# Performance work log

Measured on AMD Instinct MI355X. Metric: run time of the kernel, lower is better.

## Reference

```python
import jax, jax.numpy as jnp
import numpy as np

H = 4          # num attention heads
C1 = 64        # channel_num[0]
C2 = 128       # channel_num[1]
KV = C1 + C2   # 192
MLP = C1 * 4   # expand_ratio=4


def _layernorm(x, g, b, eps=1e-6):
    m = jnp.mean(x, axis=-1, keepdims=True)
    v = jnp.mean((x - m) ** 2, axis=-1, keepdims=True)
    return (x - m) * jax.lax.rsqrt(v + eps) * g + b


def setup_inputs() -> dict:
    key = jax.random.key(0)
    ks = jax.random.split(key, 12)
    B, N = 8, 3136
    s_q = 1.0 / np.sqrt(C1)
    s_kv = 1.0 / np.sqrt(KV)
    return {
        "emb1": jax.random.normal(ks[0], (B, N, C1), jnp.float32),
        "emb2": jax.random.normal(ks[1], (B, N, C2), jnp.float32),
        # per-head projection weights (nn.Linear convention: y = x @ W.T)
        "Wq": jax.random.uniform(ks[2], (H, C1, C1), jnp.float32, -s_q, s_q),
        "Wk": jax.random.uniform(ks[3], (H, KV, KV), jnp.float32, -s_kv, s_kv),
        "Wv": jax.random.uniform(ks[4], (H, KV, KV), jnp.float32, -s_kv, s_kv),
        "Wout": jax.random.uniform(ks[5], (C1, C1), jnp.float32, -s_q, s_q),
        "ln1_g": jnp.ones((C1,), jnp.float32),
        "ln1_b": jnp.zeros((C1,), jnp.float32),
        "lnall_g": jnp.ones((KV,), jnp.float32),
        "lnall_b": jnp.zeros((KV,), jnp.float32),
        "ffn_g": jnp.ones((C1,), jnp.float32),
        "ffn_b": jnp.zeros((C1,), jnp.float32),
        "fc1_w": jax.random.uniform(ks[6], (MLP, C1), jnp.float32, -s_q, s_q),
        "fc1_b": jnp.zeros((MLP,), jnp.float32),
        "fc2_w": jax.random.uniform(ks[7], (C1, MLP), jnp.float32, -1.0 / np.sqrt(MLP), 1.0 / np.sqrt(MLP)),
        "fc2_b": jnp.zeros((C1,), jnp.float32),
    }


def reference(emb1, emb2, Wq, Wk, Wv, Wout, ln1_g, ln1_b, lnall_g, lnall_b,
              ffn_g, ffn_b, fc1_w, fc1_b, fc2_w, fc2_b):
    # emb1: [B,N,C1], emb2: [B,N,C2]
    emb_all = jnp.concatenate([emb1, emb2], axis=2)          # [B,N,KV]
    cx1 = _layernorm(emb1, ln1_g, ln1_b)                     # [B,N,C1]
    ea = _layernorm(emb_all, lnall_g, lnall_b)               # [B,N,KV]

    # batched per-head projections (replaces Python loop over ModuleList)
    qT = jnp.einsum('bnc,hdc->bhdn', cx1, Wq)                # [B,H,C1,N]
    k = jnp.einsum('bnk,hdk->bhnd', ea, Wk)                  # [B,H,N,KV]
    vT = jnp.einsum('bnk,hdk->bhdn', ea, Wv)                 # [B,H,KV,N]

    scores = jnp.einsum('bhcn,bhnk->bhck', qT, k) / np.sqrt(KV)  # [B,H,C1,KV]
    # InstanceNorm2d over spatial dims (C1, KV) per (batch, head), affine=False
    m = jnp.mean(scores, axis=(2, 3), keepdims=True)
    v = jnp.mean((scores - m) ** 2, axis=(2, 3), keepdims=True)
    scores = (scores - m) * jax.lax.rsqrt(v + 1e-5)
    probs = jax.nn.softmax(scores, axis=3)                   # softmax over KV

    ctx = jnp.einsum('bhck,bhkn->bhcn', probs, vT)           # [B,H,C1,N]
    ctx = jnp.mean(ctx, axis=1).transpose(0, 2, 1)           # mean over heads -> [B,N,C1]
    o = ctx @ Wout.T                                         # [B,N,C1]

    cx = emb1 + o                                            # residual
    x = _layernorm(cx, ffn_g, ffn_b)
    x = jax.nn.gelu(x @ fc1_w.T + fc1_b, approximate=False)
    x = x @ fc2_w.T + fc2_b
    return x + cx
```

## Files before the change

kernel.cpp:

```cpp
#include <hip/hip_runtime.h>
#include <hip/hip_bf16.h>

typedef __hip_bfloat16 bf;
typedef unsigned short ushort_t;
typedef __attribute__((ext_vector_type(8))) short short8;
typedef __attribute__((ext_vector_type(4))) float f32x4;

#define NB 8
#define SEQ 3136
#define HD 4
#define ZS 6

__device__ __forceinline__ float lo_bf(unsigned u){ return __uint_as_float(u << 16); }
__device__ __forceinline__ float hi_bf(unsigned u){ return __uint_as_float(u & 0xffff0000u); }
__device__ __forceinline__ float b16f(ushort_t s){ return __uint_as_float(((unsigned)s) << 16); }
__device__ __forceinline__ unsigned short f2bfbits(float f){
  unsigned u = __float_as_uint(f);
  unsigned r = u + 0x7fffu + ((u >> 16) & 1u);
  return (unsigned short)(r >> 16);
}
__device__ __forceinline__ float ldin(const void* p, long i, bool isbf){
  return isbf ? __bfloat162float(((const bf*)p)[i]) : ((const float*)p)[i];
}
__device__ __forceinline__ ushort_t cvt1(const void* p, long i, bool isbf){
  return isbf ? ((const ushort_t*)p)[i] : f2bfbits(((const float*)p)[i]);
}
#define DTYPE_FLAG(p) (((const unsigned*)(p))[0] == 0x3F803F80u)

__device__ __forceinline__ float wsum(float v){
  #pragma unroll
  for (int o = 32; o > 0; o >>= 1) v += __shfl_xor(v, o, 64);
  return v;
}

__global__ __launch_bounds__(512) void k_g(
    const void* __restrict__ emb1, const void* __restrict__ emb2,
    const void* __restrict__ g1, const void* __restrict__ b1,
    const void* __restrict__ ga, const void* __restrict__ ba,
    const void* __restrict__ Wq, const void* __restrict__ Wk, const void* __restrict__ Wv,
    const void* __restrict__ f1w, const void* __restrict__ f2w, const void* __restrict__ Wout,
    ushort_t* __restrict__ part, ushort_t* __restrict__ eag,
    ushort_t* __restrict__ Wqb, ushort_t* __restrict__ Wkb, ushort_t* __restrict__ WvTb,
    ushort_t* __restrict__ f1wb, ushort_t* __restrict__ f2wb,
    ushort_t* __restrict__ Woutb, unsigned* __restrict__ cnt){
  bool isbf = DTYPE_FLAG(g1);
  int tid = threadIdx.x;
  int b = blockIdx.y, ch = blockIdx.x;
  if (ch >= 49){
    if (b != 0) return;
    int g = (ch - 49)*512 + tid;
    const int STR = 24*512;
    if (g < 8) cnt[g] = 0;
    for (int i = g; i < 16384; i += STR) Wqb[i] = cvt1(Wq, i, isbf);
    for (int i = g; i < 4096;  i += STR) Woutb[i] = cvt1(Wout, i, isbf);
    for (int i = g; i < 147456; i += STR) Wkb[i] = cvt1(Wk, i, isbf);
    for (int i = g; i < 147456; i += STR){
      int hh = i / 36864, r = i - hh*36864;
      int j = r / 192, e = r - j*192;
      WvTb[i] = cvt1(Wv, (long)hh*36864 + e*192 + j, isbf);
    }
    for (int i = g; i < 16384; i += STR) f1wb[i] = cvt1(f1w, i, isbf);
    for (int i = g; i < 16384; i += STR) f2wb[i] = cvt1(f2w, i, isbf);
    return;
  }
  __shared__ __align__(16) ushort_t z1t[64*72];
  __shared__ __align__(16) ushort_t zat[192*72];
  int wave = tid >> 6, lane = tid & 63;
  int quad = lane >> 4, nl = lane & 15;
  long t0 = (long)b*SEQ + ch*64;
  float g1l = ldin(g1,lane,isbf), b1l = ldin(b1,lane,isbf);
  float ga0 = ldin(ga,lane,isbf),     ba0 = ldin(ba,lane,isbf);
  float ga1 = ldin(ga,64+lane,isbf),  ba1 = ldin(ba,64+lane,isbf);
  float ga2 = ldin(ga,128+lane,isbf), ba2 = ldin(ba,128+lane,isbf);
  #pragma unroll 4
  for (int k = 0; k < 8; ++k){
    int tok = wave*8 + k;
    long t = t0 + tok;
    float e1  = ldin(emb1, t*64 + lane, isbf);
    float e2a = ldin(emb2, t*128 + lane, isbf);
    float e2b = ldin(emb2, t*128 + 64 + lane, isbf);
    float s1 = wsum(e1), ss1 = wsum(e1*e1);
    float m1 = s1*(1.f/64.f);
    float r1 = rsqrtf(fmaxf(ss1*(1.f/64.f) - m1*m1, 0.f) + 1e-6f);
    z1t[lane*72 + tok] = f2bfbits((e1 - m1)*r1*g1l + b1l);
    float s23 = wsum(e2a+e2b), ss23 = wsum(e2a*e2a + e2b*e2b);
    float ma = (s1+s23)*(1.f/192.f);
    float ra = rsqrtf(fmaxf((ss1+ss23)*(1.f/192.f) - ma*ma, 0.f) + 1e-6f);
    unsigned short za0 = f2bfbits((e1  - ma)*ra*ga0 + ba0);
    unsigned short za1 = f2bfbits((e2a - ma)*ra*ga1 + ba1);
    unsigned short za2 = f2bfbits((e2b - ma)*ra*ga2 + ba2);
    zat[lane*72 + tok]       = za0;
    zat[(64+lane)*72 + tok]  = za1;
    zat[(128+lane)*72 + tok] = za2;
    eag[t*192 + lane]       = za0;
    eag[t*192 + 64 + lane]  = za1;
    eag[t*192 + 128 + lane] = za2;
  }
  __syncthreads();
  int half = wave >> 2, cq = wave & 3;
  short8 a0 = *reinterpret_cast<const short8*>(&z1t[(cq*16+nl)*72 + quad*8]);
  short8 a1 = *reinterpret_cast<const short8*>(&z1t[(cq*16+nl)*72 + 32 + quad*8]);
  ushort_t* P = part + ((long)b*49 + ch)*12288;
  #pragma unroll
  for (int ntl = 0; ntl < 6; ++ntl){
    int nt = half*6 + ntl;
    f32x4 cd = {0.f,0.f,0.f,0.f};
    short8 b0 = *reinterpret_cast<const short8*>(&zat[(nt*16+nl)*72 + quad*8]);
    cd = __builtin_amdgcn_mfma_f32_16x16x32_bf16(a0, b0, cd, 0, 0, 0);
    short8 b1v = *reinterpret_cast<const short8*>(&zat[(nt*16+nl)*72 + 32 + quad*8]);
    cd = __builtin_amdgcn_mfma_f32_16x16x32_bf16(a1, b1v, cd, 0, 0, 0);
    #pragma unroll
    for (int reg = 0; reg < 4; ++reg)
      P[(cq*16 + quad*4 + reg)*192 + nt*16 + nl] = f2bfbits(cd[reg]);
  }
}

__global__ __launch_bounds__(64) void k_red(
    const ushort_t* __restrict__ part, ushort_t* __restrict__ Gb){
  int idx4 = blockIdx.x*64 + threadIdx.x;
  int b = idx4 / 3072, e4 = idx4 - b*3072;
  const ushort_t* p = part + (long)b*49*12288 + e4*4;
  float s0=0.f, s1=0.f, s2=0.f, s3=0.f;
  #pragma unroll
  for (int ch = 0; ch < 49; ++ch){
    uint2 u = *reinterpret_cast<const uint2*>(p + (long)ch*12288);
    s0 += lo_bf(u.x); s1 += hi_bf(u.x); s2 += lo_bf(u.y); s3 += hi_bf(u.y);
  }
  unsigned lo = (unsigned)f2bfbits(s0) | ((unsigned)f2bfbits(s1) << 16);
  unsigned hi = (unsigned)f2bfbits(s2) | ((unsigned)f2bfbits(s3) << 16);
  *reinterpret_cast<uint2*>(Gb + (long)idx4*4) = make_uint2(lo, hi);
}

__global__ __launch_bounds__(256) void k_att(
    const ushort_t* __restrict__ Gb, const ushort_t* __restrict__ Wqb,
    const ushort_t* __restrict__ Wkb, const ushort_t* __restrict__ WvTb,
    const ushort_t* __restrict__ Woutb,
    float* __restrict__ Mh, unsigned* __restrict__ cnt, ushort_t* __restrict__ W2){
  __shared__ __align__(16) ushort_t sT[192*72];
  __shared__ __align__(16) ushort_t sPh[64*200];
  __shared__ __align__(16) ushort_t sPl[64*200];
  __shared__ float red[8];
  __shared__ float stat[2];
  __shared__ unsigned sOld;
  int h = blockIdx.x, b = blockIdx.y, z = blockIdx.z;
  int tid = threadIdx.x, wave = tid >> 6, lane = tid & 63;
  int quad = lane >> 4, nl = lane & 15;

  const ushort_t* Gp = Gb + (long)b*12288;
  short8 aG[6];
  #pragma unroll
  for (int ks = 0; ks < 6; ++ks)
    aG[ks] = *reinterpret_cast<const short8*>(Gp + (wave*16+nl)*192 + ks*32 + quad*8);
  const ushort_t* Wkp = Wkb + (long)h*36864;
  short8 bcur[6], bnxt[6];
  #pragma unroll
  for (int ks = 0; ks < 6; ++ks)
    bcur[ks] = *reinterpret_cast<const short8*>(Wkp + (long)nl*192 + ks*32 + quad*8);
  #pragma unroll
  for (int nt = 0; nt < 12; ++nt){
    if (nt < 11){
      #pragma unroll
      for (int ks = 0; ks < 6; ++ks)
        bnxt[ks] = *reinterpret_cast<const short8*>(Wkp + (long)((nt+1)*16+nl)*192 + ks*32 + quad*8);
    }
    f32x4 cd = {0.f,0.f,0.f,0.f};
    #pragma unroll
    for (int ks = 0; ks < 6; ++ks)
      cd = __builtin_amdgcn_mfma_f32_16x16x32_bf16(aG[ks], bcur[ks], cd, 0, 0, 0);
    #pragma unroll
    for (int reg = 0; reg < 4; ++reg)
      sT[(nt*16+nl)*72 + wave*16 + quad*4 + reg] = f2bfbits(cd[reg]);
    #pragma unroll
    for (int ks = 0; ks < 6; ++ks) bcur[ks] = bnxt[ks];
  }
  __syncthreads();

  const ushort_t* Wqp = Wqb + (long)h*4096;
  short8 aQ[2];
  #pragma unroll
  for (int ks = 0; ks < 2; ++ks)
    aQ[ks] = *reinterpret_cast<const short8*>(Wqp + (wave*16+nl)*64 + ks*32 + quad*8);
  const float scale = 0.07216878364870323f;
  float sv[12][4];
  float ps = 0.f, pss = 0.f;
  #pragma unroll
  for (int nt = 0; nt < 12; ++nt){
    f32x4 cd = {0.f,0.f,0.f,0.f};
    #pragma unroll
    for (int ks = 0; ks < 2; ++ks){
      short8 bt = *reinterpret_cast<const short8*>(&sT[(nt*16+nl)*72 + ks*32 + quad*8]);
      cd = __builtin_amdgcn_mfma_f32_16x16x32_bf16(aQ[ks], bt, cd, 0, 0, 0);
    }
    #pragma unroll
    for (int reg = 0; reg < 4; ++reg){
      float v = cd[reg]*scale;
      sv[nt][reg] = v;
      ps += v; pss += v*v;
    }
  }
  ps = wsum(ps); pss = wsum(pss);
  if (lane == 0){ red[wave] = ps; red[4+wave] = pss; }
  __syncthreads();
  if (tid == 0){
    float s  = red[0]+red[1]+red[2]+red[3];
    float s2 = red[4]+red[5]+red[6]+red[7];
    float m = s * (1.f/12288.f);
    stat[0] = m;
    stat[1] = rsqrtf(fmaxf(s2*(1.f/12288.f) - m*m, 0.f) + 1e-5f);
  }
  __syncthreads();

  const ushort_t* Wvp = WvTb + (long)h*36864;
  short8 bv[2][6];
  #pragma unroll
  for (int ntl = 0; ntl < 2; ++ntl)
    #pragma unroll
    for (int ks = 0; ks < 6; ++ks)
      bv[ntl][ks] = *reinterpret_cast<const short8*>(Wvp + (long)((z*2+ntl)*16+nl)*192 + ks*32 + quad*8);

  float m = stat[0], r = stat[1];
  #pragma unroll
  for (int reg = 0; reg < 4; ++reg){
    float mx = -3.4e38f;
    #pragma unroll
    for (int nt = 0; nt < 12; ++nt){
      float v = (sv[nt][reg] - m)*r;
      sv[nt][reg] = v;
      mx = fmaxf(mx, v);
    }
    #pragma unroll
    for (int o = 1; o < 16; o <<= 1) mx = fmaxf(mx, __shfl_xor(mx, o, 64));
    float sum = 0.f;
    #pragma unroll
    for (int nt = 0; nt < 12; ++nt){
      float e = __expf(sv[nt][reg] - mx);
      sv[nt][reg] = e;
      sum += e;
    }
    #pragma unroll
    for (int o = 1; o < 16; o <<= 1) sum += __shfl_xor(sum, o, 64);
    float inv = 1.f / sum;
    int row = wave*16 + quad*4 + reg;
    #pragma unroll
    for (int nt = 0; nt < 12; ++nt){
      float e = sv[nt][reg]*inv;
      ushort_t hi = f2bfbits(e);
      sPh[row*200 + nt*16 + nl] = hi;
      sPl[row*200 + nt*16 + nl] = f2bfbits(e - b16f(hi));
    }
  }
  __syncthreads();

  short8 aPh[6], aPl[6];
  #pragma unroll
  for (int ks = 0; ks < 6; ++ks){
    aPh[ks] = *reinterpret_cast<const short8*>(&sPh[(wave*16+nl)*200 + ks*32 + quad*8]);
    aPl[ks] = *reinterpret_cast<const short8*>(&sPl[(wave*16+nl)*200 + ks*32 + quad*8]);
  }
  float* Mb = Mh + ((long)b*HD + h)*12288;
  #pragma unroll
  for (int ntl = 0; ntl < 2; ++ntl){
    int nt = z*2 + ntl;
    f32x4 cdh = {0.f,0.f,0.f,0.f};
    f32x4 cdl = {0.f,0.f,0.f,0.f};
    #pragma unroll
    for (int ks = 0; ks < 6; ++ks){
      cdl = __builtin_amdgcn_mfma_f32_16x16x32_bf16(aPl[ks], bv[ntl][ks], cdl, 0, 0, 0);
      cdh = __builtin_amdgcn_mfma_f32_16x16x32_bf16(aPh[ks], bv[ntl][ks], cdh, 0, 0, 0);
    }
    #pragma unroll
    for (int reg = 0; reg < 4; ++reg)
      Mb[(wave*16 + quad*4 + reg)*192 + nt*16 + nl] = cdh[reg] + cdl[reg];
  }

  __threadfence();
  if (tid == 0) sOld = atomicAdd(&cnt[b], 1u);
  __syncthreads();
  if (sOld == HD*ZS - 1u){
    __threadfence();
    const float* M0 = Mh + (long)b*HD*12288;
    for (int g = tid; g < 3072; g += 256){
      float4 x0 = ((const float4*)M0)[g];
      float4 x1 = ((const float4*)(M0 + 12288))[g];
      float4 x2 = ((const float4*)(M0 + 24576))[g];
      float4 x3 = ((const float4*)(M0 + 36864))[g];
      int e = g*4; int c = e/192, j = e - c*192;
      sT[(j+0)*72 + c] = f2bfbits(0.25f*(x0.x+x1.x+x2.x+x3.x));
      sT[(j+1)*72 + c] = f2bfbits(0.25f*(x0.y+x1.y+x2.y+x3.y));
      sT[(j+2)*72 + c] = f2bfbits(0.25f*(x0.z+x1.z+x2.z+x3.z));
      sT[(j+3)*72 + c] = f2bfbits(0.25f*(x0.w+x1.w+x2.w+x3.w));
    }
    __syncthreads();
    short8 aW[2];
    #pragma unroll
    for (int ks = 0; ks < 2; ++ks)
      aW[ks] = *reinterpret_cast<const short8*>(Woutb + (wave*16+nl)*64 + ks*32 + quad*8);
    ushort_t* W2b = W2 + (long)b*12288;
    #pragma unroll
    for (int nt = 0; nt < 12; ++nt){
      f32x4 cd = {0.f,0.f,0.f,0.f};
      #pragma unroll
      for (int ks = 0; ks < 2; ++ks){
        short8 bm = *reinterpret_cast<const short8*>(&sT[(nt*16+nl)*72 + ks*32 + quad*8]);
        cd = __builtin_amdgcn_mfma_f32_16x16x32_bf16(aW[ks], bm, cd, 0, 0, 0);
      }
      #pragma unroll
      for (int reg = 0; reg < 4; ++reg)
        W2b[(wave*16 + quad*4 + reg)*192 + nt*16 + nl] = f2bfbits(cd[reg]);
    }
  }
}

__global__ __launch_bounds__(256) void k_tail(
    const void* __restrict__ emb1, const ushort_t* __restrict__ eag,
    const ushort_t* __restrict__ W2g,
    const void* __restrict__ ffg, const void* __restrict__ ffb,
    const ushort_t* __restrict__ f1wb, const void* __restrict__ f1b,
    const ushort_t* __restrict__ f2wb, const void* __restrict__ f2b,
    const void* __restrict__ lng, void* __restrict__ out){
  bool isbf = DTYPE_FLAG(lng);
  __shared__ __align__(16) ushort_t sCX[16*72];
  __shared__ __align__(16) ushort_t sX[16*88];
  __shared__ __align__(16) ushort_t sH[16*280];
  int tid = threadIdx.x, wave = tid >> 6, lane = tid & 63;
  int quad = lane >> 4, nl = lane & 15;
  int b = blockIdx.y;
  long tbase = (long)b*SEQ + blockIdx.x*16;

  short8 aO[6];
  #pragma unroll
  for (int kt = 0; kt < 6; ++kt)
    aO[kt] = *reinterpret_cast<const short8*>(eag + (tbase + nl)*192 + kt*32 + quad*8);
  const ushort_t* W2b = W2g + (long)b*12288;
  {
    f32x4 cd = {0.f,0.f,0.f,0.f};
    #pragma unroll
    for (int kt = 0; kt < 6; ++kt){
      short8 bf8 = *reinterpret_cast<const short8*>(W2b + (wave*16+nl)*192 + kt*32 + quad*8);
      cd = __builtin_amdgcn_mfma_f32_16x16x32_bf16(aO[kt], bf8, cd, 0, 0, 0);
    }
    #pragma unroll
    for (int reg = 0; reg < 4; ++reg){
      int tokl = quad*4 + reg;
      int chn = wave*16 + nl;
      float e1v = ldin(emb1, (tbase + tokl)*64 + chn, isbf);
      sCX[tokl*72 + chn] = f2bfbits(cd[reg] + e1v);
    }
  }
  __syncthreads();

  float gl = ldin(ffg, lane, isbf), bl = ldin(ffb, lane, isbf);
  #pragma unroll
  for (int k = 0; k < 4; ++k){
    int tokl = wave*4 + k;
    float c = b16f(sCX[tokl*72 + lane]);
    float s = wsum(c), ss = wsum(c*c);
    float m = s*(1.f/64.f);
    float r = rsqrtf(fmaxf(ss*(1.f/64.f) - m*m, 0.f) + 1e-6f);
    sX[tokl*88 + lane] = f2bfbits((c - m)*r*gl + bl);
  }
  __syncthreads();

  short8 aX[2];
  #pragma unroll
  for (int kt = 0; kt < 2; ++kt)
    aX[kt] = *reinterpret_cast<const short8*>(&sX[nl*88 + kt*32 + quad*8]);
  #pragma unroll
  for (int nn = 0; nn < 4; ++nn){
    int nt = wave*4 + nn;
    f32x4 cd = {0.f,0.f,0.f,0.f};
    #pragma unroll
    for (int kt = 0; kt < 2; ++kt){
      short8 bf8 = *reinterpret_cast<const short8*>(f1wb + (long)(nt*16+nl)*64 + kt*32 + quad*8);
      cd = __builtin_amdgcn_mfma_f32_16x16x32_bf16(aX[kt], bf8, cd, 0, 0, 0);
    }
    float bb = ldin(f1b, nt*16+nl, isbf);
    #pragma unroll
    for (int reg = 0; reg < 4; ++reg){
      float v = cd[reg] + bb;
      float h = 0.5f*v*(1.f + erff(v*0.70710678118654752f));
      sH[(quad*4 + reg)*280 + nt*16 + nl] = f2bfbits(h);
    }
  }
  __syncthreads();

  short8 aH[8];
  #pragma unroll
  for (int kt = 0; kt < 8; ++kt)
    aH[kt] = *reinterpret_cast<const short8*>(&sH[nl*280 + kt*32 + quad*8]);
  {
    f32x4 cd = {0.f,0.f,0.f,0.f};
    #pragma unroll
    for (int kt = 0; kt < 8; ++kt){
      short8 bf8 = *reinterpret_cast<const short8*>(f2wb + (long)(wave*16+nl)*256 + kt*32 + quad*8);
      cd = __builtin_amdgcn_mfma_f32_16x16x32_bf16(aH[kt], bf8, cd, 0, 0, 0);
    }
    float bb2 = ldin(f2b, wave*16+nl, isbf);
    #pragma unroll
    for (int reg = 0; reg < 4; ++reg){
      int tokl = quad*4 + reg;
      int chn = wave*16 + nl;
      float y = cd[reg] + bb2 + b16f(sCX[tokl*72 + chn]);
      if (isbf) sCX[tokl*72 + chn] = f2bfbits(y);
      else ((float*)out)[(tbase + tokl)*64 + chn] = y;
    }
  }
  if (isbf){
    __syncthreads();
    int tokl = wave*4 + (lane >> 4), prt = lane & 15;
    uint2 v = *reinterpret_cast<const uint2*>(&sCX[tokl*72 + prt*4]);
    *reinterpret_cast<uint2*>((ushort_t*)out + (tbase + tokl)*64 + prt*4) = v;
  }
}

extern "C" void kernel_launch(void* const* d_in, const int* in_sizes, int n_in,
                              void* d_out, int out_size, void* d_ws, size_t ws_size,
                              hipStream_t stream){
  const void* emb1 = d_in[0];
  const void* emb2 = d_in[1];
  const void* Wq   = d_in[2];
  const void* Wk   = d_in[3];
  const void* Wv   = d_in[4];
  const void* Wout = d_in[5];
  const void* ln1g = d_in[6];
  const void* ln1b = d_in[7];
  const void* lag  = d_in[8];
  const void* lab  = d_in[9];
  const void* ffg  = d_in[10];
  const void* ffb  = d_in[11];
  const void* f1w  = d_in[12];
  const void* f1b  = d_in[13];
  const void* f2w  = d_in[14];
  const void* f2b  = d_in[15];

  char* base = (char*)d_ws;
  ushort_t* part = (ushort_t*)base;
  ushort_t* ea   = (ushort_t*)(base + 9633792);
  ushort_t* Gb   = (ushort_t*)(base + 19267584);
  float*    Mh   = (float*)(base + 19464192);
  ushort_t* W2   = (ushort_t*)(base + 21037056);
  ushort_t* Wqb  = (ushort_t*)(base + 21233664);
  ushort_t* Wkb  = (ushort_t*)(base + 21266432);
  ushort_t* WvTb = (ushort_t*)(base + 21561344);
  ushort_t* f1wb = (ushort_t*)(base + 21856256);
  ushort_t* f2wb = (ushort_t*)(base + 21889024);
  ushort_t* Woutb= (ushort_t*)(base + 21921792);
  unsigned* cnt  = (unsigned*)(base + 21929984);

  k_g   <<<dim3(73,NB),     512, 0, stream>>>(emb1, emb2, ln1g, ln1b, lag, lab,
                                              Wq, Wk, Wv, f1w, f2w, Wout,
                                              part, ea, Wqb, Wkb, WvTb, f1wb, f2wb,
                                              Woutb, cnt);
  k_red <<<384,              64, 0, stream>>>(part, Gb);
  k_att <<<dim3(HD,NB,ZS),  256, 0, stream>>>(Gb, Wqb, Wkb, WvTb, Woutb, Mh, cnt, W2);
  k_tail<<<dim3(196,NB),    256, 0, stream>>>(emb1, ea, W2, ffg, ffb,
                                              f1wb, f1b, f2wb, f2b, ln1g, d_out);
}
```

Before: 183.1 us.

## Split Wout projection out of attention kernel into separate k_w2 launch

```diff
diff --git a/kernel.cpp b/kernel.cpp
--- a/kernel.cpp
+++ b/kernel.cpp
@@ -22,6 +22,14 @@
 __device__ __forceinline__ float ldin(const void* p, long i, bool isbf){
   return isbf ? __bfloat162float(((const bf*)p)[i]) : ((const float*)p)[i];
 }
+__device__ __forceinline__ float4 ld4(const void* p, long i, bool isbf){
+  if (isbf){
+    uint2 u = *reinterpret_cast<const uint2*>((const unsigned short*)p + i);
+    return make_float4(lo_bf(u.x), hi_bf(u.x), lo_bf(u.y), hi_bf(u.y));
+  }
+  const float* f = (const float*)p + i;
+  return make_float4(f[0], f[1], f[2], f[3]);
+}
 __device__ __forceinline__ ushort_t cvt1(const void* p, long i, bool isbf){
   return isbf ? ((const ushort_t*)p)[i] : f2bfbits(((const float*)p)[i]);
 }
@@ -38,11 +46,10 @@
     const void* __restrict__ g1, const void* __restrict__ b1,
     const void* __restrict__ ga, const void* __restrict__ ba,
     const void* __restrict__ Wq, const void* __restrict__ Wk, const void* __restrict__ Wv,
-    const void* __restrict__ f1w, const void* __restrict__ f2w, const void* __restrict__ Wout,
+    const void* __restrict__ f1w, const void* __restrict__ f2w,
     ushort_t* __restrict__ part, ushort_t* __restrict__ eag,
     ushort_t* __restrict__ Wqb, ushort_t* __restrict__ Wkb, ushort_t* __restrict__ WvTb,
-    ushort_t* __restrict__ f1wb, ushort_t* __restrict__ f2wb,
-    ushort_t* __restrict__ Woutb, unsigned* __restrict__ cnt){
+    ushort_t* __restrict__ f1wb, ushort_t* __restrict__ f2wb){
   bool isbf = DTYPE_FLAG(g1);
   int tid = threadIdx.x;
   int b = blockIdx.y, ch = blockIdx.x;
@@ -50,9 +57,7 @@
     if (b != 0) return;
     int g = (ch - 49)*512 + tid;
     const int STR = 24*512;
-    if (g < 8) cnt[g] = 0;
     for (int i = g; i < 16384; i += STR) Wqb[i] = cvt1(Wq, i, isbf);
-    for (int i = g; i < 4096;  i += STR) Woutb[i] = cvt1(Wout, i, isbf);
     for (int i = g; i < 147456; i += STR) Wkb[i] = cvt1(Wk, i, isbf);
     for (int i = g; i < 147456; i += STR){
       int hh = i / 36864, r = i - hh*36864;
@@ -134,14 +139,12 @@
 __global__ __launch_bounds__(256) void k_att(
     const ushort_t* __restrict__ Gb, const ushort_t* __restrict__ Wqb,
     const ushort_t* __restrict__ Wkb, const ushort_t* __restrict__ WvTb,
-    const ushort_t* __restrict__ Woutb,
-    float* __restrict__ Mh, unsigned* __restrict__ cnt, ushort_t* __restrict__ W2){
+    float* __restrict__ Mh){
   __shared__ __align__(16) ushort_t sT[192*72];
   __shared__ __align__(16) ushort_t sPh[64*200];
   __shared__ __align__(16) ushort_t sPl[64*200];
   __shared__ float red[8];
   __shared__ float stat[2];
-  __shared__ unsigned sOld;
   int h = blockIdx.x, b = blockIdx.y, z = blockIdx.z;
   int tid = threadIdx.x, wave = tid >> 6, lane = tid & 63;
   int quad = lane >> 4, nl = lane & 15;
@@ -272,43 +275,50 @@
     for (int reg = 0; reg < 4; ++reg)
       Mb[(wave*16 + quad*4 + reg)*192 + nt*16 + nl] = cdh[reg] + cdl[reg];
   }
-
-  __threadfence();
-  if (tid == 0) sOld = atomicAdd(&cnt[b], 1u);
-  __syncthreads();
-  if (sOld == HD*ZS - 1u){
-    __threadfence();
-    const float* M0 = Mh + (long)b*HD*12288;
-    for (int g = tid; g < 3072; g += 256){
-      float4 x0 = ((const float4*)M0)[g];
-      float4 x1 = ((const float4*)(M0 + 12288))[g];
-      float4 x2 = ((const float4*)(M0 + 24576))[g];
-      float4 x3 = ((const float4*)(M0 + 36864))[g];
-      int e = g*4; int c = e/192, j = e - c*192;
-      sT[(j+0)*72 + c] = f2bfbits(0.25f*(x0.x+x1.x+x2.x+x3.x));
-      sT[(j+1)*72 + c] = f2bfbits(0.25f*(x0.y+x1.y+x2.y+x3.y));
-      sT[(j+2)*72 + c] = f2bfbits(0.25f*(x0.z+x1.z+x2.z+x3.z));
-      sT[(j+3)*72 + c] = f2bfbits(0.25f*(x0.w+x1.w+x2.w+x3.w));
-    }
-    __syncthreads();
-    short8 aW[2];
-    #pragma unroll
-    for (int ks = 0; ks < 2; ++ks)
-      aW[ks] = *reinterpret_cast<const short8*>(Woutb + (wave*16+nl)*64 + ks*32 + quad*8);
-    ushort_t* W2b = W2 + (long)b*12288;
-    #pragma unroll
-    for (int nt = 0; nt < 12; ++nt){
-      f32x4 cd = {0.f,0.f,0.f,0.f};
+}
+
+__global__ __launch_bounds__(256) void k_w2(
+    const float* __restrict__ Mh, const void* __restrict__ Wout,
+    const void* __restrict__ lng, ushort_t* __restrict__ W2){
+  bool isbf = DTYPE_FLAG(lng);
+  __shared__ __align__(16) float sM[64*49];
+  int jc = blockIdx.x, b = blockIdx.y;
+  int tid = threadIdx.x;
+  for (int idx = tid; idx < 3072; idx += 256){
+    int c = idx/48, j = idx - c*48;
+    long base = (long)b*HD*12288 + c*192 + jc*48 + j;
+    float s = Mh[base] + Mh[base+12288] + Mh[base+2*12288] + Mh[base+3*12288];
+    sM[c*49 + j] = 0.25f*s;
+  }
+  __syncthreads();
+  int ty = tid >> 4, tx = tid & 15;
+  float acc[4][3];
+  #pragma unroll
+  for (int i=0;i<4;++i) for (int q=0;q<3;++q) acc[i][q]=0.f;
+  for (int c = 0; c < 64; c += 4){
+    float4 w4[4];
+    #pragma unroll
+    for (int i=0;i<4;++i) w4[i] = ld4(Wout, (long)(ty*4+i)*64 + c, isbf);
+    float ww[4][4];
+    #pragma unroll
+    for (int i=0;i<4;++i){ ww[i][0]=w4[i].x; ww[i][1]=w4[i].y; ww[i][2]=w4[i].z; ww[i][3]=w4[i].w; }
+    #pragma unroll
+    for (int u = 0; u < 4; ++u){
+      float t3[3];
       #pragma unroll
-      for (int ks = 0; ks < 2; ++ks){
-        short8 bm = *reinterpret_cast<const short8*>(&sT[(nt*16+nl)*72 + ks*32 + quad*8]);
-        cd = __builtin_amdgcn_mfma_f32_16x16x32_bf16(aW[ks], bm, cd, 0, 0, 0);
-      }
+      for (int q=0;q<3;++q) t3[q] = sM[(c+u)*49 + tx*3 + q];
       #pragma unroll
-      for (int reg = 0; reg < 4; ++reg)
-        W2b[(wave*16 + quad*4 + reg)*192 + nt*16 + nl] = f2bfbits(cd[reg]);
-    }
-  }
+      for (int i=0;i<4;++i)
+        #pragma unroll
+        for (int q=0;q<3;++q) acc[i][q] = fmaf(ww[i][u], t3[q], acc[i][q]);
+    }
+  }
+  ushort_t* W2b = W2 + (long)b*12288;
+  #pragma unroll
+  for (int i=0;i<4;++i)
+    #pragma unroll
+    for (int q=0;q<3;++q)
+      W2b[(ty*4+i)*192 + jc*48 + tx*3 + q] = f2bfbits(acc[i][q]);
 }
 
 __global__ __launch_bounds__(256) void k_tail(
@@ -444,15 +454,13 @@
   ushort_t* WvTb = (ushort_t*)(base + 21561344);
   ushort_t* f1wb = (ushort_t*)(base + 21856256);
   ushort_t* f2wb = (ushort_t*)(base + 21889024);
-  ushort_t* Woutb= (ushort_t*)(base + 21921792);
-  unsigned* cnt  = (unsigned*)(base + 21929984);
 
   k_g   <<<dim3(73,NB),     512, 0, stream>>>(emb1, emb2, ln1g, ln1b, lag, lab,
-                                              Wq, Wk, Wv, f1w, f2w, Wout,
-                                              part, ea, Wqb, Wkb, WvTb, f1wb, f2wb,
-                                              Woutb, cnt);
+                                              Wq, Wk, Wv, f1w, f2w,
+                                              part, ea, Wqb, Wkb, WvTb, f1wb, f2wb);
   k_red <<<384,              64, 0, stream>>>(part, Gb);
-  k_att <<<dim3(HD,NB,ZS),  256, 0, stream>>>(Gb, Wqb, Wkb, WvTb, Woutb, Mh, cnt, W2);
+  k_att <<<dim3(HD,NB,ZS),  256, 0, stream>>>(Gb, Wqb, Wkb, WvTb, Mh);
+  k_w2  <<<dim3(4,NB),      256, 0, stream>>>(Mh, Wout, ln1g, W2);
   k_tail<<<dim3(196,NB),    256, 0, stream>>>(emb1, ea, W2, ffg, ffb,
                                               f1wb, f1b, f2wb, f2b, ln1g, d_out);
 }
```

New measurement: 169.9 us. 7.2% less time.
